# Kernel optimization log

Measured on AMD Instinct MI355X. Metric: run time of the kernel, lower is better.

Reference implementation:

```python
import jax, jax.numpy as jnp
import numpy as np

H = 16
D_MODEL = 1024
D_K = D_MODEL // H
NEG_INF = -1e9


def setup_inputs() -> dict:
    key = jax.random.key(0)
    ks = jax.random.split(key, 11)
    B, S = 4, 2048
    scale = 1.0 / np.sqrt(D_MODEL)
    inp = {
        "query": jax.random.normal(ks[0], (B, S, D_MODEL), jnp.float32),
        "key": jax.random.normal(ks[1], (B, S, D_MODEL), jnp.float32),
        "value": jax.random.normal(ks[2], (B, S, D_MODEL), jnp.float32),
        "Wq": jax.random.normal(ks[3], (D_MODEL, D_MODEL), jnp.float32) * scale,
        "bq": jnp.zeros((D_MODEL,), jnp.float32),
        "Wk": jax.random.normal(ks[4], (D_MODEL, D_MODEL), jnp.float32) * scale,
        "bk": jnp.zeros((D_MODEL,), jnp.float32),
        "Wv": jax.random.normal(ks[5], (D_MODEL, D_MODEL), jnp.float32) * scale,
        "bv": jnp.zeros((D_MODEL,), jnp.float32),
        "Wo": jax.random.normal(ks[6], (D_MODEL, D_MODEL), jnp.float32) * scale,
        "bo": jnp.zeros((D_MODEL,), jnp.float32),
    }
    return inp


def _split_heads(x):
    # [B, S, D] -> [B, H, S, D_K]
    B, S, _ = x.shape
    return x.reshape(B, S, H, D_K).transpose(0, 2, 1, 3)


def reference(query, key, value, Wq, bq, Wk, bk, Wv, bv, Wo, bo):
    # Linear projections (torch Linear: y = x @ W.T + b)
    q = _split_heads(query @ Wq.T + bq)   # [B,H,S,Dk]
    k = _split_heads(key @ Wk.T + bk)
    v = _split_heads(value @ Wv.T + bv)

    S = q.shape[2]
    scores = jnp.einsum("bhqd,bhkd->bhqk", q, k) / jnp.sqrt(jnp.float32(D_K))
    causal = jnp.tril(jnp.ones((S, S), jnp.bool_))  # [S,S]
    scores = jnp.where(causal[None, None], scores, NEG_INF)
    p_attn = jax.nn.softmax(scores, axis=-1)  # dropout p=0.0 (eval)
    x = jnp.einsum("bhqk,bhkd->bhqd", p_attn, v)  # [B,H,S,Dk]
    B = x.shape[0]
    x = x.transpose(0, 2, 1, 3).reshape(B, S, H * D_K)
    return x @ Wo.T + bo
```

## Files before the change

### kernel.cpp

```cpp
#include <hip/hip_runtime.h>
#include <hip/hip_bf16.h>
#include <stdint.h>

#define NH 16
#define SEQ 2048
#define DMODEL 1024
#define DK 64
#define BATCH 4
#define M_TOT 8192

#define LOG2E 1.44269504088896f
#define QSCALE (0.125f * LOG2E)

typedef short v8bf __attribute__((ext_vector_type(8)));
typedef float f32x4 __attribute__((ext_vector_type(4)));

__device__ __forceinline__ unsigned short f2bf(float f) {
  union { float f; unsigned u; } v; v.f = f;
  return (unsigned short)((v.u + 0x7fffu + ((v.u >> 16) & 1u)) >> 16);
}

__device__ __forceinline__ unsigned pack_bf2(float a, float b) {
  return (unsigned)f2bf(a) | ((unsigned)f2bf(b) << 16);
}

__device__ __forceinline__ void async_load16(const void* g, void* l) {
  __builtin_amdgcn_global_load_lds(
      (const __attribute__((address_space(1))) unsigned int*)(uintptr_t)g,
      (__attribute__((address_space(3))) unsigned int*)(unsigned)(uintptr_t)l,
      16, 0, 0);
}

__global__ __launch_bounds__(256)
void cvt_kernel(const float* __restrict__ q, const float* __restrict__ k,
                const float* __restrict__ v,
                const float* __restrict__ wq, const float* __restrict__ wk,
                const float* __restrict__ wv, const float* __restrict__ wo,
                unsigned short* __restrict__ oq, unsigned short* __restrict__ ok,
                unsigned short* __restrict__ ov,
                unsigned short* __restrict__ owq, unsigned short* __restrict__ owk,
                unsigned short* __restrict__ owv, unsigned short* __restrict__ owo)
{
  const size_t XN = (size_t)M_TOT * DMODEL;
  const size_t WN = (size_t)DMODEL * DMODEL;
  const float* s; unsigned short* d; size_t n;
  switch (blockIdx.y) {
    case 0: s = q;  d = oq;  n = XN; break;
    case 1: s = k;  d = ok;  n = XN; break;
    case 2: s = v;  d = ov;  n = XN; break;
    case 3: s = wq; d = owq; n = WN; break;
    case 4: s = wk; d = owk; n = WN; break;
    case 5: s = wv; d = owv; n = WN; break;
    default: s = wo; d = owo; n = WN; break;
  }
  for (size_t i = ((size_t)blockIdx.x * 256 + threadIdx.x) * 8; i < n;
       i += (size_t)gridDim.x * 256 * 8) {
    float4 a = *(const float4*)(s + i);
    float4 b = *(const float4*)(s + i + 4);
    uint4 p = { pack_bf2(a.x, a.y), pack_bf2(a.z, a.w),
                pack_bf2(b.x, b.y), pack_bf2(b.z, b.w) };
    *(uint4*)(d + i) = p;
  }
}

__global__ __launch_bounds__(256, 2)
void proj_bf16_kernel(const unsigned short* __restrict__ Xq,
                      const unsigned short* __restrict__ Xk,
                      const unsigned short* __restrict__ Xv,
                      const unsigned short* __restrict__ Wqc,
                      const unsigned short* __restrict__ Wkc,
                      const unsigned short* __restrict__ Wvc,
                      const float* __restrict__ bq, const float* __restrict__ bk,
                      const float* __restrict__ bv,
                      unsigned short* __restrict__ Qp, unsigned short* __restrict__ Kp,
                      unsigned short* __restrict__ Vp)
{
  const int z = blockIdx.z;
  const unsigned short* A = (z == 0) ? Xq : (z == 1) ? Xk : Xv;
  const unsigned short* W = (z == 0) ? Wqc : (z == 1) ? Wkc : Wvc;
  const float* bias = (z == 0) ? bq : (z == 1) ? bk : bv;
  unsigned short* Out = (z == 0) ? Qp : (z == 1) ? Kp : Vp;
  const float scale = (z == 0) ? QSCALE : 1.0f;

  __shared__ unsigned short As[128 * 64];
  __shared__ unsigned short Bs[128 * 64];

  const int tid  = threadIdx.x;
  const int m0   = blockIdx.x * 128;
  const int n0   = blockIdx.y * 128;
  const int lane = tid & 63;
  const int wave = tid >> 6;
  const int quad = lane >> 4;
  const int l16  = lane & 15;
  const int wm   = (wave >> 1) * 64;
  const int wn   = (wave & 1) * 64;
  const int lrow = lane >> 3;
  const int lcol = lane & 7;

  f32x4 acc[4][4];
#pragma unroll
  for (int i = 0; i < 4; ++i)
#pragma unroll
    for (int j = 0; j < 4; ++j) acc[i][j] = (f32x4){0.f, 0.f, 0.f, 0.f};

  for (int k0 = 0; k0 < DMODEL; k0 += 64) {
#pragma unroll
    for (int i = 0; i < 4; ++i) {
      int row = wave * 32 + i * 8 + lrow;
      int gc = (lcol ^ (row & 7)) * 8;
      async_load16(A + (size_t)(m0 + row) * DMODEL + k0 + gc, &As[(wave * 32 + i * 8) * 64]);
      async_load16(W + (size_t)(n0 + row) * DMODEL + k0 + gc, &Bs[(wave * 32 + i * 8) * 64]);
    }
    __syncthreads();

#pragma unroll
    for (int ks = 0; ks < 2; ++ks) {
      v8bf af[4], bf[4];
#pragma unroll
      for (int i = 0; i < 4; ++i)
        af[i] = *(const v8bf*)&As[(wm + i * 16 + l16) * 64 + ((ks * 4 + quad) ^ (l16 & 7)) * 8];
#pragma unroll
      for (int j = 0; j < 4; ++j)
        bf[j] = *(const v8bf*)&Bs[(wn + j * 16 + l16) * 64 + ((ks * 4 + quad) ^ (l16 & 7)) * 8];
#pragma unroll
      for (int i = 0; i < 4; ++i)
#pragma unroll
        for (int j = 0; j < 4; ++j)
          acc[i][j] = __builtin_amdgcn_mfma_f32_16x16x32_bf16(af[i], bf[j], acc[i][j], 0, 0, 0);
    }
    __syncthreads();
  }

  if (z < 2) {
#pragma unroll
    for (int j = 0; j < 4; ++j) {
      int colg = n0 + wn + j * 16 + l16;
      float bj = bias[colg];
      int h = colg >> 6, d = colg & 63;
#pragma unroll
      for (int i = 0; i < 4; ++i) {
#pragma unroll
        for (int reg = 0; reg < 4; ++reg) {
          int mrow = m0 + wm + i * 16 + quad * 4 + reg;
          int bb = mrow >> 11, ss = mrow & 2047;
          float val = (acc[i][j][reg] + bj) * scale;
          Out[(((size_t)bb * NH + h) * SEQ + ss) * DK + d] = f2bf(val);
        }
      }
    }
  } else {
#pragma unroll
    for (int j = 0; j < 4; ++j) {
      int colg = n0 + wn + j * 16 + l16;
      float bj = bias[colg];
      int h = colg >> 6, d = colg & 63;
#pragma unroll
      for (int i = 0; i < 4; ++i) {
        int mrow = m0 + wm + i * 16 + quad * 4;
        int bb = mrow >> 11, ss = mrow & 2047;
        uint2 pk = { pack_bf2(acc[i][j][0] + bj, acc[i][j][1] + bj),
                     pack_bf2(acc[i][j][2] + bj, acc[i][j][3] + bj) };
        *(uint2*)(Out + (((size_t)bb * NH + h) * DK + d) * SEQ + ss) = pk;
      }
    }
  }
}

__global__ __launch_bounds__(256, 2)
void attn_kernel(const unsigned short* __restrict__ Qp,
                 const unsigned short* __restrict__ Kp,
                 const unsigned short* __restrict__ VTp,
                 unsigned short* __restrict__ Xout)
{
  const int y  = blockIdx.y;
  const int qt = (y & 1) ? (y >> 1) : (15 - (y >> 1));
  const int bh = blockIdx.x;
  const int b  = bh >> 4, h = bh & 15;

  const unsigned short* Qb = Qp  + ((size_t)bh * SEQ + qt * 128) * DK;
  const unsigned short* Kb = Kp  + (size_t)bh * SEQ * DK;
  const unsigned short* Vb = VTp + (size_t)bh * DK * SEQ;

  __shared__ unsigned short Ks[2][64 * 64];
  __shared__ unsigned short VTs[2][64 * 64];
  __shared__ unsigned short Ps[4][16 * 64];

  const int tid  = threadIdx.x;
  const int lane = tid & 63, wave = tid >> 6;
  const int quad = lane >> 4, l16 = lane & 15;
  const int row_lo = qt * 128 + wave * 32;

  v8bf qf[2][2];
#pragma unroll
  for (int rf = 0; rf < 2; ++rf)
#pragma unroll
    for (int ks = 0; ks < 2; ++ks)
      qf[rf][ks] = *(const v8bf*)(Qb + (size_t)(wave * 32 + rf * 16 + l16) * DK + ks * 32 + quad * 8);

  float lp[2][4];
  f32x4 o[2][4];
#pragma unroll
  for (int rf = 0; rf < 2; ++rf)
#pragma unroll
    for (int reg = 0; reg < 4; ++reg) lp[rf][reg] = 0.f;
#pragma unroll
  for (int rf = 0; rf < 2; ++rf)
#pragma unroll
    for (int df = 0; df < 4; ++df) o[rf][df] = (f32x4){0.f, 0.f, 0.f, 0.f};

  const int nchunk = 2 * (qt + 1);
  const int lrow = lane >> 3;
  const int lcol = lane & 7;

#pragma unroll
  for (int is = 0; is < 2; ++is) {
    int row = wave * 16 + is * 8 + lrow;
    int cK = ((lcol ^ (row & 7)) * 8);
    async_load16(Kb + (size_t)row * DK + cK, &Ks[0][(wave * 16 + is * 8) * 64]);
    async_load16(Vb + (size_t)row * SEQ + cK, &VTs[0][(wave * 16 + is * 8) * 64]);
  }
  __syncthreads();

  for (int c = 0; c < nchunk; ++c) {
    const int buf = c & 1;
    const int kb  = c * 64;

    if (c + 1 < nchunk) {
      const int kb2 = kb + 64;
#pragma unroll
      for (int is = 0; is < 2; ++is) {
        int row = wave * 16 + is * 8 + lrow;
        int cc = ((lcol ^ (row & 7)) * 8);
        async_load16(Kb + (size_t)(kb2 + row) * DK + cc, &Ks[buf ^ 1][(wave * 16 + is * 8) * 64]);
        async_load16(Vb + (size_t)row * SEQ + kb2 + cc, &VTs[buf ^ 1][(wave * 16 + is * 8) * 64]);
      }
    }

    if (kb <= row_lo + 31) {
      f32x4 s[2][4];
#pragma unroll
      for (int rf = 0; rf < 2; ++rf)
#pragma unroll
        for (int nf = 0; nf < 4; ++nf) s[rf][nf] = (f32x4){0.f, 0.f, 0.f, 0.f};
#pragma unroll
      for (int ks = 0; ks < 2; ++ks)
#pragma unroll
        for (int nf = 0; nf < 4; ++nf) {
          v8bf kf = *(const v8bf*)&Ks[buf][(nf * 16 + l16) * 64 + ((ks * 4 + quad) ^ (l16 & 7)) * 8];
          s[0][nf] = __builtin_amdgcn_mfma_f32_16x16x32_bf16(qf[0][ks], kf, s[0][nf], 0, 0, 0);
          s[1][nf] = __builtin_amdgcn_mfma_f32_16x16x32_bf16(qf[1][ks], kf, s[1][nf], 0, 0, 0);
        }

      if (kb + 63 > row_lo) {
#pragma unroll
        for (int rf = 0; rf < 2; ++rf)
#pragma unroll
          for (int nf = 0; nf < 4; ++nf) {
            int col = kb + nf * 16 + l16;
#pragma unroll
            for (int reg = 0; reg < 4; ++reg)
              if (col > row_lo + rf * 16 + quad * 4 + reg) s[rf][nf][reg] = -1e30f;
          }
      }

#pragma unroll
      for (int rf = 0; rf < 2; ++rf) {
#pragma unroll
        for (int nf = 0; nf < 4; ++nf)
#pragma unroll
          for (int reg = 0; reg < 4; ++reg)
            s[rf][nf][reg] = __builtin_amdgcn_exp2f(s[rf][nf][reg]);
#pragma unroll
        for (int reg = 0; reg < 4; ++reg)
          lp[rf][reg] += (s[rf][0][reg] + s[rf][1][reg]) + (s[rf][2][reg] + s[rf][3][reg]);

#pragma unroll
        for (int nf = 0; nf < 4; ++nf)
#pragma unroll
          for (int reg = 0; reg < 4; ++reg)
            Ps[wave][(quad * 4 + reg) * 64 +
                     (((nf * 2 + (l16 >> 3)) ^ (quad * 2)) * 8) + (l16 & 7)] =
                f2bf(s[rf][nf][reg]);

#pragma unroll
        for (int ks = 0; ks < 2; ++ks) {
          v8bf pf = *(const v8bf*)&Ps[wave][l16 * 64 + (((ks * 4 + quad) ^ ((l16 >> 2) * 2)) * 8)];
#pragma unroll
          for (int df = 0; df < 4; ++df) {
            v8bf vf = *(const v8bf*)&VTs[buf][(df * 16 + l16) * 64 + ((ks * 4 + quad) ^ (l16 & 7)) * 8];
            o[rf][df] = __builtin_amdgcn_mfma_f32_16x16x32_bf16(pf, vf, o[rf][df], 0, 0, 0);
          }
        }
      }
    }
    __syncthreads();
  }

#pragma unroll
  for (int rf = 0; rf < 2; ++rf) {
#pragma unroll
    for (int off = 1; off < 16; off <<= 1)
#pragma unroll
      for (int reg = 0; reg < 4; ++reg) lp[rf][reg] += __shfl_xor(lp[rf][reg], off);
    float inv[4];
#pragma unroll
    for (int reg = 0; reg < 4; ++reg) inv[reg] = 1.0f / lp[rf][reg];
#pragma unroll
    for (int df = 0; df < 4; ++df)
#pragma unroll
      for (int reg = 0; reg < 4; ++reg) {
        int qrow = row_lo + rf * 16 + quad * 4 + reg;
        Xout[(size_t)(b * SEQ + qrow) * DMODEL + h * DK + df * 16 + l16] =
            f2bf(o[rf][df][reg] * inv[reg]);
      }
  }
}

__global__ __launch_bounds__(256, 2)
void oproj_kernel(const unsigned short* __restrict__ Xa,
                  const unsigned short* __restrict__ Woc,
                  const float* __restrict__ bo,
                  float* __restrict__ Out)
{
  __shared__ unsigned short As[128 * 64];
  __shared__ unsigned short Bs[128 * 64];

  const int tid  = threadIdx.x;
  const int m0   = blockIdx.x * 128;
  const int n0   = blockIdx.y * 128;
  const int lane = tid & 63;
  const int wave = tid >> 6;
  const int quad = lane >> 4;
  const int l16  = lane & 15;
  const int wm   = (wave >> 1) * 64;
  const int wn   = (wave & 1) * 64;
  const int lrow = lane >> 3;
  const int lcol = lane & 7;

  f32x4 acc[4][4];
#pragma unroll
  for (int i = 0; i < 4; ++i)
#pragma unroll
    for (int j = 0; j < 4; ++j) acc[i][j] = (f32x4){0.f, 0.f, 0.f, 0.f};

  for (int k0 = 0; k0 < DMODEL; k0 += 64) {
#pragma unroll
    for (int i = 0; i < 4; ++i) {
      int row = wave * 32 + i * 8 + lrow;
      int gc = (lcol ^ (row & 7)) * 8;
      async_load16(Xa  + (size_t)(m0 + row) * DMODEL + k0 + gc, &As[(wave * 32 + i * 8) * 64]);
      async_load16(Woc + (size_t)(n0 + row) * DMODEL + k0 + gc, &Bs[(wave * 32 + i * 8) * 64]);
    }
    __syncthreads();

#pragma unroll
    for (int ks = 0; ks < 2; ++ks) {
      v8bf af[4], bf[4];
#pragma unroll
      for (int i = 0; i < 4; ++i)
        af[i] = *(const v8bf*)&As[(wm + i * 16 + l16) * 64 + ((ks * 4 + quad) ^ (l16 & 7)) * 8];
#pragma unroll
      for (int j = 0; j < 4; ++j)
        bf[j] = *(const v8bf*)&Bs[(wn + j * 16 + l16) * 64 + ((ks * 4 + quad) ^ (l16 & 7)) * 8];
#pragma unroll
      for (int i = 0; i < 4; ++i)
#pragma unroll
        for (int j = 0; j < 4; ++j)
          acc[i][j] = __builtin_amdgcn_mfma_f32_16x16x32_bf16(af[i], bf[j], acc[i][j], 0, 0, 0);
    }
    __syncthreads();
  }

#pragma unroll
  for (int j = 0; j < 4; ++j) {
    int colg = n0 + wn + j * 16 + l16;
    float bj = bo[colg];
#pragma unroll
    for (int i = 0; i < 4; ++i) {
#pragma unroll
      for (int reg = 0; reg < 4; ++reg) {
        int mrow = m0 + wm + i * 16 + quad * 4 + reg;
        Out[(size_t)mrow * DMODEL + colg] = acc[i][j][reg] + bj;
      }
    }
  }
}

extern "C" void kernel_launch(void* const* d_in, const int* in_sizes, int n_in,
                              void* d_out, int out_size, void* d_ws, size_t ws_size,
                              hipStream_t stream)
{
  const float* query = (const float*)d_in[0];
  const float* key   = (const float*)d_in[1];
  const float* value = (const float*)d_in[2];
  const float* Wq = (const float*)d_in[3];
  const float* bq = (const float*)d_in[4];
  const float* Wk = (const float*)d_in[5];
  const float* bk = (const float*)d_in[6];
  const float* Wv = (const float*)d_in[7];
  const float* bv = (const float*)d_in[8];
  const float* Wo = (const float*)d_in[9];
  const float* bo = (const float*)d_in[10];

  const size_t tsz = (size_t)M_TOT * DMODEL;
  const size_t wsz = (size_t)DMODEL * DMODEL;
  unsigned short* Qp  = (unsigned short*)d_ws;
  unsigned short* Kp  = Qp + tsz;
  unsigned short* Vp  = Kp + tsz;
  unsigned short* Xa  = Vp + tsz;
  unsigned short* Xqc = Xa + tsz;
  unsigned short* Xkc = Xqc + tsz;
  unsigned short* Xvc = Xkc + tsz;
  unsigned short* Wqc = Xvc + tsz;
  unsigned short* Wkc = Wqc + wsz;
  unsigned short* Wvc = Wkc + wsz;
  unsigned short* Woc = Wvc + wsz;

  cvt_kernel<<<dim3(1024, 7), 256, 0, stream>>>(query, key, value, Wq, Wk, Wv, Wo,
                                                Xqc, Xkc, Xvc, Wqc, Wkc, Wvc, Woc);
  proj_bf16_kernel<<<dim3(64, 8, 3), 256, 0, stream>>>(Xqc, Xkc, Xvc, Wqc, Wkc, Wvc,
                                                       bq, bk, bv, Qp, Kp, Vp);
  attn_kernel<<<dim3(64, 16), 256, 0, stream>>>(Qp, Kp, Vp, Xa);
  oproj_kernel<<<dim3(64, 8), 256, 0, stream>>>(Xa, Woc, bo, (float*)d_out);
}
```

Baseline: 312.7 us.

## Stage projection epilogue through LDS, load attention K/V directly, raise occupancy

The projection epilogue now writes results into the reused shared-memory tiles with a swizzle, then reads them back and issues 16-byte coalesced global stores instead of scattered 2-byte and 8-byte stores. The attention kernel drops the shared-memory double-buffered K/V staging and its block barriers. Each wave reads K and V fragments straight from global memory and loops only over the chunks it needs, so waves no longer wait on each other. Launch bounds for all three GEMM/attention kernels rise from 2 to 3 blocks per CU, which caps registers per thread. This risks redundant global/L2 traffic for K/V, since every wave reloads the same tiles, and possible register spills.

```diff
diff --git a/kernel.cpp b/kernel.cpp
--- a/kernel.cpp
+++ b/kernel.cpp
@@ -63,7 +63,7 @@
   }
 }
 
-__global__ __launch_bounds__(256, 2)
+__global__ __launch_bounds__(256, 3)
 void proj_bf16_kernel(const unsigned short* __restrict__ Xq,
                       const unsigned short* __restrict__ Xk,
                       const unsigned short* __restrict__ Xv,
@@ -131,42 +131,61 @@
     __syncthreads();
   }
 
+  unsigned short* Ew = (wave < 2) ? (As + wave * 4096) : (Bs + (wave - 2) * 4096);
+
   if (z < 2) {
 #pragma unroll
     for (int j = 0; j < 4; ++j) {
       int colg = n0 + wn + j * 16 + l16;
       float bj = bias[colg];
-      int h = colg >> 6, d = colg & 63;
-#pragma unroll
-      for (int i = 0; i < 4; ++i) {
+#pragma unroll
+      for (int i = 0; i < 4; ++i)
 #pragma unroll
         for (int reg = 0; reg < 4; ++reg) {
-          int mrow = m0 + wm + i * 16 + quad * 4 + reg;
-          int bb = mrow >> 11, ss = mrow & 2047;
-          float val = (acc[i][j][reg] + bj) * scale;
-          Out[(((size_t)bb * NH + h) * SEQ + ss) * DK + d] = f2bf(val);
+          int ml = i * 16 + quad * 4 + reg;
+          Ew[ml * 64 + (((j * 2 + (l16 >> 3)) ^ (ml & 7)) * 8) + (l16 & 7)] =
+              f2bf((acc[i][j][reg] + bj) * scale);
         }
-      }
+    }
+#pragma unroll
+    for (int r = 0; r < 8; ++r) {
+      int ml = r * 8 + (lane >> 3);
+      uint4 val = *(const uint4*)&Ew[ml * 64 + (((lane & 7) ^ (lane >> 3)) * 8)];
+      int mrow = m0 + wm + ml;
+      int bb = mrow >> 11, ss = mrow & 2047;
+      int colg0 = n0 + wn + (lane & 7) * 8;
+      int hh = colg0 >> 6, dd = colg0 & 63;
+      *(uint4*)(Out + (((size_t)bb * NH + hh) * SEQ + ss) * DK + dd) = val;
     }
   } else {
 #pragma unroll
     for (int j = 0; j < 4; ++j) {
       int colg = n0 + wn + j * 16 + l16;
       float bj = bias[colg];
-      int h = colg >> 6, d = colg & 63;
-#pragma unroll
-      for (int i = 0; i < 4; ++i) {
-        int mrow = m0 + wm + i * 16 + quad * 4;
-        int bb = mrow >> 11, ss = mrow & 2047;
-        uint2 pk = { pack_bf2(acc[i][j][0] + bj, acc[i][j][1] + bj),
-                     pack_bf2(acc[i][j][2] + bj, acc[i][j][3] + bj) };
-        *(uint2*)(Out + (((size_t)bb * NH + h) * DK + d) * SEQ + ss) = pk;
-      }
-    }
-  }
-}
-
-__global__ __launch_bounds__(256, 2)
+      int nl = j * 16 + l16;
+#pragma unroll
+      for (int i = 0; i < 4; ++i)
+#pragma unroll
+        for (int reg = 0; reg < 4; ++reg) {
+          int ml = i * 16 + quad * 4 + reg;
+          Ew[nl * 64 + (((ml >> 3) ^ (nl & 7)) * 8) + (ml & 7)] =
+              f2bf(acc[i][j][reg] + bj);
+        }
+    }
+#pragma unroll
+    for (int r = 0; r < 8; ++r) {
+      int nl = r * 8 + (lane >> 3);
+      uint4 val = *(const uint4*)&Ew[nl * 64 + (((lane & 7) ^ (lane >> 3)) * 8)];
+      int colg = n0 + wn + nl;
+      int hh = colg >> 6, dd = colg & 63;
+      int mrow0 = m0 + wm + (lane & 7) * 8;
+      int bb = mrow0 >> 11, ss = mrow0 & 2047;
+      *(uint4*)(Out + (((size_t)bb * NH + hh) * DK + dd) * SEQ + ss) = val;
+    }
+  }
+}
+
+__global__ __launch_bounds__(256, 3)
 void attn_kernel(const unsigned short* __restrict__ Qp,
                  const unsigned short* __restrict__ Kp,
                  const unsigned short* __restrict__ VTp,
@@ -181,9 +200,7 @@
   const unsigned short* Kb = Kp  + (size_t)bh * SEQ * DK;
   const unsigned short* Vb = VTp + (size_t)bh * DK * SEQ;
 
-  __shared__ unsigned short Ks[2][64 * 64];
-  __shared__ unsigned short VTs[2][64 * 64];
-  __shared__ unsigned short Ps[4][16 * 64];
+  __shared__ unsigned short Ps[4][32 * 64];
 
   const int tid  = threadIdx.x;
   const int lane = tid & 63, wave = tid >> 6;
@@ -208,92 +225,71 @@
 #pragma unroll
     for (int df = 0; df < 4; ++df) o[rf][df] = (f32x4){0.f, 0.f, 0.f, 0.f};
 
-  const int nchunk = 2 * (qt + 1);
-  const int lrow = lane >> 3;
-  const int lcol = lane & 7;
-
-#pragma unroll
-  for (int is = 0; is < 2; ++is) {
-    int row = wave * 16 + is * 8 + lrow;
-    int cK = ((lcol ^ (row & 7)) * 8);
-    async_load16(Kb + (size_t)row * DK + cK, &Ks[0][(wave * 16 + is * 8) * 64]);
-    async_load16(Vb + (size_t)row * SEQ + cK, &VTs[0][(wave * 16 + is * 8) * 64]);
-  }
-  __syncthreads();
-
-  for (int c = 0; c < nchunk; ++c) {
-    const int buf = c & 1;
-    const int kb  = c * 64;
-
-    if (c + 1 < nchunk) {
-      const int kb2 = kb + 64;
-#pragma unroll
-      for (int is = 0; is < 2; ++is) {
-        int row = wave * 16 + is * 8 + lrow;
-        int cc = ((lcol ^ (row & 7)) * 8);
-        async_load16(Kb + (size_t)(kb2 + row) * DK + cc, &Ks[buf ^ 1][(wave * 16 + is * 8) * 64]);
-        async_load16(Vb + (size_t)row * SEQ + kb2 + cc, &VTs[buf ^ 1][(wave * 16 + is * 8) * 64]);
+  const int cmax = (row_lo + 31) >> 6;
+
+  for (int c = 0; c <= cmax; ++c) {
+    const int kb = c * 64;
+
+    f32x4 s[2][4];
+#pragma unroll
+    for (int rf = 0; rf < 2; ++rf)
+#pragma unroll
+      for (int nf = 0; nf < 4; ++nf) s[rf][nf] = (f32x4){0.f, 0.f, 0.f, 0.f};
+#pragma unroll
+    for (int ks = 0; ks < 2; ++ks)
+#pragma unroll
+      for (int nf = 0; nf < 4; ++nf) {
+        v8bf kf = *(const v8bf*)(Kb + (size_t)(kb + nf * 16 + l16) * DK + ks * 32 + quad * 8);
+        s[0][nf] = __builtin_amdgcn_mfma_f32_16x16x32_bf16(qf[0][ks], kf, s[0][nf], 0, 0, 0);
+        s[1][nf] = __builtin_amdgcn_mfma_f32_16x16x32_bf16(qf[1][ks], kf, s[1][nf], 0, 0, 0);
       }
-    }
-
-    if (kb <= row_lo + 31) {
-      f32x4 s[2][4];
+
+    if (kb + 63 > row_lo) {
 #pragma unroll
       for (int rf = 0; rf < 2; ++rf)
 #pragma unroll
-        for (int nf = 0; nf < 4; ++nf) s[rf][nf] = (f32x4){0.f, 0.f, 0.f, 0.f};
+        for (int nf = 0; nf < 4; ++nf) {
+          int col = kb + nf * 16 + l16;
+#pragma unroll
+          for (int reg = 0; reg < 4; ++reg)
+            if (col > row_lo + rf * 16 + quad * 4 + reg) s[rf][nf][reg] = -1e30f;
+        }
+    }
+
+#pragma unroll
+    for (int rf = 0; rf < 2; ++rf) {
+#pragma unroll
+      for (int nf = 0; nf < 4; ++nf)
+#pragma unroll
+        for (int reg = 0; reg < 4; ++reg)
+          s[rf][nf][reg] = __builtin_amdgcn_exp2f(s[rf][nf][reg]);
+#pragma unroll
+      for (int reg = 0; reg < 4; ++reg)
+        lp[rf][reg] += (s[rf][0][reg] + s[rf][1][reg]) + (s[rf][2][reg] + s[rf][3][reg]);
+#pragma unroll
+      for (int nf = 0; nf < 4; ++nf)
+#pragma unroll
+        for (int reg = 0; reg < 4; ++reg)
+          Ps[wave][(rf * 16 + quad * 4 + reg) * 64 +
+                   (((nf * 2 + (l16 >> 3)) ^ (quad * 2)) * 8) + (l16 & 7)] =
+              f2bf(s[rf][nf][reg]);
+    }
+
+    v8bf pf[2][2];
+#pragma unroll
+    for (int rf = 0; rf < 2; ++rf)
 #pragma unroll
       for (int ks = 0; ks < 2; ++ks)
-#pragma unroll
-        for (int nf = 0; nf < 4; ++nf) {
-          v8bf kf = *(const v8bf*)&Ks[buf][(nf * 16 + l16) * 64 + ((ks * 4 + quad) ^ (l16 & 7)) * 8];
-          s[0][nf] = __builtin_amdgcn_mfma_f32_16x16x32_bf16(qf[0][ks], kf, s[0][nf], 0, 0, 0);
-          s[1][nf] = __builtin_amdgcn_mfma_f32_16x16x32_bf16(qf[1][ks], kf, s[1][nf], 0, 0, 0);
-        }
-
-      if (kb + 63 > row_lo) {
-#pragma unroll
-        for (int rf = 0; rf < 2; ++rf)
-#pragma unroll
-          for (int nf = 0; nf < 4; ++nf) {
-            int col = kb + nf * 16 + l16;
-#pragma unroll
-            for (int reg = 0; reg < 4; ++reg)
-              if (col > row_lo + rf * 16 + quad * 4 + reg) s[rf][nf][reg] = -1e30f;
-          }
+        pf[rf][ks] = *(const v8bf*)&Ps[wave][(rf * 16 + l16) * 64 +
+                                            (((ks * 4 + quad) ^ ((l16 >> 2) * 2)) * 8)];
+#pragma unroll
+    for (int ks = 0; ks < 2; ++ks)
+#pragma unroll
+      for (int df = 0; df < 4; ++df) {
+        v8bf vf = *(const v8bf*)(Vb + (size_t)(df * 16 + l16) * SEQ + kb + ks * 32 + quad * 8);
+        o[0][df] = __builtin_amdgcn_mfma_f32_16x16x32_bf16(pf[0][ks], vf, o[0][df], 0, 0, 0);
+        o[1][df] = __builtin_amdgcn_mfma_f32_16x16x32_bf16(pf[1][ks], vf, o[1][df], 0, 0, 0);
       }
-
-#pragma unroll
-      for (int rf = 0; rf < 2; ++rf) {
-#pragma unroll
-        for (int nf = 0; nf < 4; ++nf)
-#pragma unroll
-          for (int reg = 0; reg < 4; ++reg)
-            s[rf][nf][reg] = __builtin_amdgcn_exp2f(s[rf][nf][reg]);
-#pragma unroll
-        for (int reg = 0; reg < 4; ++reg)
-          lp[rf][reg] += (s[rf][0][reg] + s[rf][1][reg]) + (s[rf][2][reg] + s[rf][3][reg]);
-
-#pragma unroll
-        for (int nf = 0; nf < 4; ++nf)
-#pragma unroll
-          for (int reg = 0; reg < 4; ++reg)
-            Ps[wave][(quad * 4 + reg) * 64 +
-                     (((nf * 2 + (l16 >> 3)) ^ (quad * 2)) * 8) + (l16 & 7)] =
-                f2bf(s[rf][nf][reg]);
-
-#pragma unroll
-        for (int ks = 0; ks < 2; ++ks) {
-          v8bf pf = *(const v8bf*)&Ps[wave][l16 * 64 + (((ks * 4 + quad) ^ ((l16 >> 2) * 2)) * 8)];
-#pragma unroll
-          for (int df = 0; df < 4; ++df) {
-            v8bf vf = *(const v8bf*)&VTs[buf][(df * 16 + l16) * 64 + ((ks * 4 + quad) ^ (l16 & 7)) * 8];
-            o[rf][df] = __builtin_amdgcn_mfma_f32_16x16x32_bf16(pf, vf, o[rf][df], 0, 0, 0);
-          }
-        }
-      }
-    }
-    __syncthreads();
   }
 
 #pragma unroll
@@ -316,7 +312,7 @@
   }
 }
 
-__global__ __launch_bounds__(256, 2)
+__global__ __launch_bounds__(256, 3)
 void oproj_kernel(const unsigned short* __restrict__ Xa,
                   const unsigned short* __restrict__ Woc,
                   const float* __restrict__ bo,
```

After: 424.2 us. 1.36x slower.
